# Kernel tuning notes

Hardware: AMD Instinct MI355X
Metric: run time of the kernel (lower is better)

Reference implementation:

```python
import jax, jax.numpy as jnp
import numpy as np

N_HEAD = 16
N_EMBD = 1024
HEAD_DIM = N_EMBD // N_HEAD
ROPE_BASE = 10000.0


def _rope_tables(T, dim):
    inv_freq = 1.0 / (ROPE_BASE ** (jnp.arange(0, dim, 2, dtype=jnp.float32) / dim))
    t = jnp.arange(T, dtype=jnp.float32)
    freqs = jnp.einsum('i,j->ij', t, inv_freq)          # [T, dim/2]
    emb = jnp.concatenate((freqs, freqs), axis=-1)       # [T, dim]
    return jnp.cos(emb), jnp.sin(emb)


def _rotate_half(x):
    x1, x2 = jnp.split(x, 2, axis=-1)
    return jnp.concatenate((-x2, x1), axis=-1)


def setup_inputs() -> dict:
    key = jax.random.key(0)
    k_x, k_wa, k_ba, k_wp, k_bp = jax.random.split(key, 5)
    B, T, C = 2, 2048, N_EMBD
    x = jax.random.normal(k_x, (B, T, C), dtype=jnp.float32)
    # torch Linear weights: [out, in]
    W_attn = jax.random.normal(k_wa, (3 * C, C), dtype=jnp.float32) * (1.0 / np.sqrt(C))
    b_attn = jax.random.normal(k_ba, (3 * C,), dtype=jnp.float32) * 0.01
    W_proj = jax.random.normal(k_wp, (C, C), dtype=jnp.float32) * (1.0 / np.sqrt(C))
    b_proj = jax.random.normal(k_bp, (C,), dtype=jnp.float32) * 0.01
    return {"x": x, "W_attn": W_attn, "b_attn": b_attn, "W_proj": W_proj, "b_proj": b_proj}


def reference(x, W_attn, b_attn, W_proj, b_proj):
    B, T, C = x.shape
    H, D = N_HEAD, HEAD_DIM
    qkv = jnp.einsum('btc,oc->bto', x, W_attn) + b_attn   # [B,T,3C]
    q, k, v = jnp.split(qkv, 3, axis=2)
    # [B,T,C] -> [B,H,T,D]
    q = q.reshape(B, T, H, D).transpose(0, 2, 1, 3)
    k = k.reshape(B, T, H, D).transpose(0, 2, 1, 3)
    v = v.reshape(B, T, H, D).transpose(0, 2, 1, 3)
    cos, sin = _rope_tables(T, D)                          # [T,D]
    q = q * cos + _rotate_half(q) * sin
    k = k * cos + _rotate_half(k) * sin
    att = jnp.einsum('bhqd,bhkd->bhqk', q, k) * (1.0 / np.sqrt(D))
    causal = jnp.tril(jnp.ones((T, T), dtype=bool))
    att = jnp.where(causal, att, -jnp.inf)
    att = jax.nn.softmax(att, axis=-1)
    y = jnp.einsum('bhqk,bhkd->bhqd', att, v)              # [B,H,T,D]
    y = y.transpose(0, 2, 1, 3).reshape(B, T, C)
    y = jnp.einsum('btc,oc->bto', y, W_proj) + b_proj
    return y
```

## Files before the change

kernel.cpp:

```cpp
#include <hip/hip_runtime.h>


typedef unsigned short u16;
typedef u16 u16x4 __attribute__((ext_vector_type(4)));
typedef u16 u16x8 __attribute__((ext_vector_type(8)));
typedef short s16x8 __attribute__((ext_vector_type(8)));
typedef float f32x4 __attribute__((ext_vector_type(4)));

#define T_SEQ 2048
#define C_EMB 1024
#define NH 16
#define HD 64

#define MFMA16(a, b, c) __builtin_amdgcn_mfma_f32_16x16x32_bf16(a, b, c, 0, 0, 0)

__device__ __forceinline__ u16 f2bf(float f) {
    union { float f; unsigned int i; } x; x.f = f;
    unsigned int r = x.i + 0x7fffu + ((x.i >> 16) & 1u);
    return (u16)(r >> 16);
}
__device__ __forceinline__ u16x4 pack4(f32x4 v) {
    u16x4 o;
#pragma unroll
    for (int j = 0; j < 4; ++j) o[j] = f2bf(v[j]);
    return o;
}

__global__ __launch_bounds__(256) void conv_k(const float* __restrict__ src, u16* __restrict__ dst, int n8) {
    int i = blockIdx.x * 256 + threadIdx.x;
    if (i >= n8) return;
    f32x4 a = ((const f32x4*)src)[i * 2];
    f32x4 b = ((const f32x4*)src)[i * 2 + 1];
    u16x8 o;
#pragma unroll
    for (int j = 0; j < 4; ++j) o[j] = f2bf(a[j]);
#pragma unroll
    for (int j = 0; j < 4; ++j) o[4 + j] = f2bf(b[j]);
    ((u16x8*)dst)[i] = o;
}

__global__ __launch_bounds__(256) void rope_tab_k(float2* __restrict__ tab) {
    int idx = blockIdx.x * 256 + threadIdx.x;
    int t = idx >> 5, j = idx & 31;
    float inv = __builtin_exp2f(-0.41524101186092f * (float)j);
    float s_, c_;
    sincosf((float)t * inv, &s_, &c_);
    tab[idx] = make_float2(c_, s_);
}

__global__ __launch_bounds__(256) void qkv_rope_k(const u16* __restrict__ xb, const u16* __restrict__ Wab,
                                                  const float* __restrict__ bias,
                                                  const float2* __restrict__ tab,
                                                  u16* __restrict__ qb, u16* __restrict__ kb,
                                                  u16* __restrict__ vt) {
    __shared__ u16 smem[2 * 128 * 72];
    u16* As = smem;
    u16* Bs = smem + 128 * 72;
    int tid = threadIdx.x;
    int n0 = blockIdx.x * 128, m0 = blockIdx.y * 128;
    int w = tid >> 6, lane = tid & 63, lr = lane & 15, quad = lane >> 4;
    int wr = w >> 1, wc = w & 1;
    f32x4 acc[4][4] = {};
    for (int kt = 0; kt < C_EMB; kt += 64) {
#pragma unroll
        for (int it = 0; it < 4; ++it) {
            int idx = it * 256 + tid;
            int row = idx >> 3, c8 = (idx & 7) << 3;
            *(s16x8*)&As[row * 72 + c8] = *(const s16x8*)(xb + (size_t)(m0 + row) * C_EMB + kt + c8);
            *(s16x8*)&Bs[row * 72 + c8] = *(const s16x8*)(Wab + (size_t)(n0 + row) * C_EMB + kt + c8);
        }
        __syncthreads();
#pragma unroll
        for (int ks = 0; ks < 64; ks += 32) {
            s16x8 af[4], bf[4];
#pragma unroll
            for (int i = 0; i < 4; ++i)
                af[i] = *(const s16x8*)&As[(wr * 64 + i * 16 + lr) * 72 + ks + quad * 8];
#pragma unroll
            for (int j = 0; j < 4; ++j)
                bf[j] = *(const s16x8*)&Bs[(wc * 64 + j * 16 + lr) * 72 + ks + quad * 8];
#pragma unroll
            for (int i = 0; i < 4; ++i)
#pragma unroll
                for (int j = 0; j < 4; ++j) acc[i][j] = MFMA16(af[i], bf[j], acc[i][j]);
        }
        __syncthreads();
    }
    int sec = n0 >> 10;
    float bv[4];
#pragma unroll
    for (int j = 0; j < 4; ++j) bv[j] = bias[n0 + wc * 64 + j * 16 + lr];

    int h0 = (n0 & 1023) >> 6;
    int b = m0 >> 11, tbase = m0 & 2047;
    if (sec == 2) {
        u16* Ct = smem;
#pragma unroll
        for (int i = 0; i < 4; ++i)
#pragma unroll
            for (int j = 0; j < 4; ++j) {
                f32x4 vv;
#pragma unroll
                for (int r = 0; r < 4; ++r) vv[r] = acc[i][j][r] + bv[j];
                int d = wc * 64 + j * 16 + lr;
                int m4 = wr * 64 + i * 16 + quad * 4;
                *(u16x4*)&Ct[d * 136 + m4] = pack4(vv);
            }
        __syncthreads();
        size_t hb = (size_t)(b * NH);
#pragma unroll
        for (int p = 0; p < 8; ++p) {
            int idx = p * 256 + tid;
            int d = idx >> 4, mc = (idx & 15) << 3;
            s16x8 vdat = *(const s16x8*)&Ct[d * 136 + mc];
            int h = h0 + (d >> 6), dd = d & 63;
            *(s16x8*)(vt + ((hb + h) * HD + dd) * T_SEQ + tbase + mc) = vdat;
        }
    } else {
        u16* dst = (sec == 0) ? qb : kb;
        float qs = (sec == 0) ? 0.18033688011112043f : 1.0f;
        u16* Ct = smem;
#pragma unroll
        for (int i = 0; i < 4; ++i)
#pragma unroll
            for (int r = 0; r < 4; ++r) {
                int mrow = wr * 64 + i * 16 + quad * 4 + r;
                int t = (m0 + mrow) & 2047;
#pragma unroll
                for (int j = 0; j < 2; ++j) {
                    int d1 = j * 16 + lr;
                    float2 cs = tab[t * 32 + d1];
                    float v1 = acc[i][j][r] + bv[j];
                    float v2 = acc[i][j + 2][r] + bv[j + 2];
                    int n1 = wc * 64 + j * 16 + lr;
                    Ct[mrow * 136 + n1]      = f2bf((v1 * cs.x - v2 * cs.y) * qs);
                    Ct[mrow * 136 + n1 + 32] = f2bf((v2 * cs.x + v1 * cs.y) * qs);
                }
            }
        __syncthreads();
#pragma unroll
        for (int p = 0; p < 8; ++p) {
            int idx = p * 256 + tid;
            int mrow = idx >> 4, c = idx & 15;
            s16x8 vdat = *(const s16x8*)&Ct[mrow * 136 + c * 8];
            int h = h0 + (c >> 3), dd = (c & 7) << 3;
            *(s16x8*)(dst + ((size_t)(b * NH + h) * T_SEQ + tbase + mrow) * HD + dd) = vdat;
        }
    }
}

__global__ __launch_bounds__(256) void flash_k(const u16* __restrict__ qb, const u16* __restrict__ kb,
                                               const u16* __restrict__ vt, u16* __restrict__ yab) {
    __shared__ u16 Ks[2][64 * 72];
    __shared__ u16 Vs[2][64 * 72];
    __shared__ u16 Ps[4][32 * 72];
    int tid = threadIdx.x;
    int bx = blockIdx.x, by = blockIdx.y;
    int qt = (by < 16) ? (15 - bx) : bx;
    int bh = by;
    int w = tid >> 6, lane = tid & 63, lr = lane & 15, quad = lane >> 4;
    int q0 = qt * 128;
    const u16* qh = qb + (size_t)bh * T_SEQ * HD;
    const u16* kh = kb + (size_t)bh * T_SEQ * HD;
    const u16* vh = vt + (size_t)bh * HD * T_SEQ;

    int rb[2];
    rb[0] = q0 + w * 16;
    rb[1] = q0 + 112 - w * 16;

    s16x8 aq[2][2];
#pragma unroll
    for (int s = 0; s < 2; ++s)
#pragma unroll
        for (int ks = 0; ks < 2; ++ks)
            aq[s][ks] = *(const s16x8*)(qh + (size_t)(rb[s] + lr) * HD + ks * 32 + quad * 8);

    int srow = tid >> 3, sc8 = (tid & 7) << 3;

    float m_i[2] = {-1e30f, -1e30f}, l_i[2] = {0.f, 0.f};
    f32x4 oacc[2][4] = {};

    int ktmax = 2 * qt + 1;
    {
        s16x8 kr0 = *(const s16x8*)(kh + (size_t)srow * HD + sc8);
        s16x8 kr1 = *(const s16x8*)(kh + (size_t)(srow + 32) * HD + sc8);
        s16x8 vr0 = *(const s16x8*)(vh + (size_t)srow * T_SEQ + sc8);
        s16x8 vr1 = *(const s16x8*)(vh + (size_t)(srow + 32) * T_SEQ + sc8);
        *(s16x8*)&Ks[0][srow * 72 + sc8] = kr0;
        *(s16x8*)&Ks[0][(srow + 32) * 72 + sc8] = kr1;
        *(s16x8*)&Vs[0][srow * 72 + sc8] = vr0;
        *(s16x8*)&Vs[0][(srow + 32) * 72 + sc8] = vr1;
    }
    __syncthreads();

    for (int kt = 0; kt <= ktmax; ++kt) {
        int cur = kt & 1;
        int k0 = kt * 64;
        bool pf = kt < ktmax;
        s16x8 kr0, kr1, vr0, vr1;
        if (pf) {
            int kn = k0 + 64;
            kr0 = *(const s16x8*)(kh + (size_t)(kn + srow) * HD + sc8);
            kr1 = *(const s16x8*)(kh + (size_t)(kn + srow + 32) * HD + sc8);
            vr0 = *(const s16x8*)(vh + (size_t)srow * T_SEQ + kn + sc8);
            vr1 = *(const s16x8*)(vh + (size_t)(srow + 32) * T_SEQ + kn + sc8);
        }
        const u16* Kc = Ks[cur];
        const u16* Vc = Vs[cur];
        s16x8 ak[2][4], av[2][4];
#pragma unroll
        for (int ks = 0; ks < 2; ++ks)
#pragma unroll
            for (int tc = 0; tc < 4; ++tc) {
                ak[ks][tc] = *(const s16x8*)&Kc[(tc * 16 + lr) * 72 + ks * 32 + quad * 8];
                av[ks][tc] = *(const s16x8*)&Vc[(tc * 16 + lr) * 72 + ks * 32 + quad * 8];
            }

#pragma unroll
        for (int s = 0; s < 2; ++s) {
            int rbase = rb[s];
            if (k0 > rbase + 15) continue;
            f32x4 sacc[4] = {};
#pragma unroll
            for (int ks = 0; ks < 2; ++ks)
#pragma unroll
                for (int tc = 0; tc < 4; ++tc) sacc[tc] = MFMA16(ak[ks][tc], aq[s][ks], sacc[tc]);
            if (k0 + 63 > rbase) {
#pragma unroll
                for (int tc = 0; tc < 4; ++tc)
#pragma unroll
                    for (int r = 0; r < 4; ++r)
                        if (k0 + tc * 16 + quad * 4 + r > rbase + lr) sacc[tc][r] = -1e30f;
            }
            f32x4 mv = sacc[0];
#pragma unroll
            for (int tc = 1; tc < 4; ++tc)
#pragma unroll
                for (int r = 0; r < 4; ++r) mv[r] = fmaxf(mv[r], sacc[tc][r]);
            float mx = fmaxf(fmaxf(mv[0], mv[1]), fmaxf(mv[2], mv[3]));
            mx = fmaxf(mx, __shfl_xor(mx, 16, 64));
            mx = fmaxf(mx, __shfl_xor(mx, 32, 64));
            float mo = m_i[s];
            bool need = !__all(mx <= mo + 8.0f);
            float alpha = 1.0f;
            if (need) {
                float mn = fmaxf(mo, mx);
                alpha = __builtin_exp2f(mo - mn);
                m_i[s] = mn;
                l_i[s] *= alpha;
            }
            float mnow = m_i[s];
            f32x4 rv = {0.f, 0.f, 0.f, 0.f};
#pragma unroll
            for (int tc = 0; tc < 4; ++tc)
#pragma unroll
                for (int r = 0; r < 4; ++r) {
                    float p = __builtin_exp2f(sacc[tc][r] - mnow);
                    sacc[tc][r] = p;
                    rv[r] += p;
                }
            float rs = (rv[0] + rv[1]) + (rv[2] + rv[3]);
            rs += __shfl_xor(rs, 16, 64);
            rs += __shfl_xor(rs, 32, 64);
            l_i[s] += rs;
#pragma unroll
            for (int tc = 0; tc < 4; ++tc)
                *(u16x4*)&Ps[w][(s * 16 + lr) * 72 + tc * 16 + quad * 4] = pack4(sacc[tc]);
            if (need) {
#pragma unroll
                for (int tn = 0; tn < 4; ++tn)
#pragma unroll
                    for (int r = 0; r < 4; ++r) oacc[s][tn][r] *= alpha;
            }
#pragma unroll
            for (int ks = 0; ks < 2; ++ks) {
                s16x8 ap = *(const s16x8*)&Ps[w][(s * 16 + lr) * 72 + ks * 32 + quad * 8];
#pragma unroll
                for (int tn = 0; tn < 4; ++tn) oacc[s][tn] = MFMA16(av[ks][tn], ap, oacc[s][tn]);
            }
        }
        if (pf) {
            int nx = cur ^ 1;
            *(s16x8*)&Ks[nx][srow * 72 + sc8] = kr0;
            *(s16x8*)&Ks[nx][(srow + 32) * 72 + sc8] = kr1;
            *(s16x8*)&Vs[nx][srow * 72 + sc8] = vr0;
            *(s16x8*)&Vs[nx][(srow + 32) * 72 + sc8] = vr1;
        }
        __syncthreads();
    }
    int b = bh >> 4, hh = bh & 15;
#pragma unroll
    for (int s = 0; s < 2; ++s) {
        float inv = 1.f / l_i[s];
        int t = rb[s] + lr;
        size_t base = ((size_t)b * T_SEQ + t) * C_EMB + hh * HD;
#pragma unroll
        for (int tn = 0; tn < 4; ++tn) {
            f32x4 vv;
#pragma unroll
            for (int r = 0; r < 4; ++r) vv[r] = oacc[s][tn][r] * inv;
            *(u16x4*)(yab + base + tn * 16 + quad * 4) = pack4(vv);
        }
    }
}

__global__ __launch_bounds__(256) void proj_k(const u16* __restrict__ ya, const u16* __restrict__ Wpb,
                                              const float* __restrict__ bias, float* __restrict__ out) {
    __shared__ u16 As[128 * 72];
    __shared__ u16 Bs[128 * 72];
    int tid = threadIdx.x;
    int n0 = blockIdx.x * 128, m0 = blockIdx.y * 128;
    int w = tid >> 6, lane = tid & 63, lr = lane & 15, quad = lane >> 4;
    int wr = w >> 1, wc = w & 1;
    f32x4 acc[4][4] = {};
    for (int kt = 0; kt < C_EMB; kt += 64) {
#pragma unroll
        for (int it = 0; it < 4; ++it) {
            int idx = it * 256 + tid;
            int row = idx >> 3, c8 = (idx & 7) << 3;
            *(s16x8*)&As[row * 72 + c8] = *(const s16x8*)(ya + (size_t)(m0 + row) * C_EMB + kt + c8);
            *(s16x8*)&Bs[row * 72 + c8] = *(const s16x8*)(Wpb + (size_t)(n0 + row) * C_EMB + kt + c8);
        }
        __syncthreads();
#pragma unroll
        for (int ks = 0; ks < 64; ks += 32) {
            s16x8 af[4], bf[4];
#pragma unroll
            for (int i = 0; i < 4; ++i)
                af[i] = *(const s16x8*)&As[(wr * 64 + i * 16 + lr) * 72 + ks + quad * 8];
#pragma unroll
            for (int j = 0; j < 4; ++j)
                bf[j] = *(const s16x8*)&Bs[(wc * 64 + j * 16 + lr) * 72 + ks + quad * 8];
#pragma unroll
            for (int i = 0; i < 4; ++i)
#pragma unroll
                for (int j = 0; j < 4; ++j) acc[i][j] = MFMA16(af[i], bf[j], acc[i][j]);
        }
        __syncthreads();
    }
    float bv[4];
#pragma unroll
    for (int j = 0; j < 4; ++j) bv[j] = bias[n0 + wc * 64 + j * 16 + lr];
#pragma unroll
    for (int i = 0; i < 4; ++i)
#pragma unroll
        for (int r = 0; r < 4; ++r) {
            int m = m0 + wr * 64 + i * 16 + quad * 4 + r;
#pragma unroll
            for (int j = 0; j < 4; ++j)
                out[(size_t)m * C_EMB + n0 + wc * 64 + j * 16 + lr] = acc[i][j][r] + bv[j];
        }
}

extern "C" void kernel_launch(void* const* d_in, const int* in_sizes, int n_in,
                              void* d_out, int out_size, void* d_ws, size_t ws_size,
                              hipStream_t stream) {
    const float *x = nullptr, *Wa = nullptr, *ba = nullptr, *Wp = nullptr, *bp = nullptr;
    for (int i = 0; i < n_in; ++i) {
        switch (in_sizes[i]) {
            case 4194304: x  = (const float*)d_in[i]; break;
            case 3145728: Wa = (const float*)d_in[i]; break;
            case 3072:    ba = (const float*)d_in[i]; break;
            case 1048576: Wp = (const float*)d_in[i]; break;
            case 1024:    bp = (const float*)d_in[i]; break;
            default: break;
        }
    }
    float* out = (float*)d_out;

    char* ws = (char*)d_ws;
    u16* qb     = (u16*)(ws);
    u16* kb     = (u16*)(ws + 8388608);
    u16* vt     = (u16*)(ws + 16777216);
    u16* yab    = (u16*)(ws + 25165824);
    float2* tab = (float2*)(ws + 33554432);
    u16* xb     = (u16*)(ws + 35651584);
    u16* Wab    = (u16*)(ws + 44040192);
    u16* Wpb    = (u16*)(ws + 50331648);

    conv_k<<<2048, 256, 0, stream>>>(x, xb, 524288);
    conv_k<<<1536, 256, 0, stream>>>(Wa, Wab, 393216);
    conv_k<<<512, 256, 0, stream>>>(Wp, Wpb, 131072);
    rope_tab_k<<<256, 256, 0, stream>>>(tab);
    qkv_rope_k<<<dim3(24, 32), 256, 0, stream>>>(xb, Wab, ba, tab, qb, kb, vt);
    flash_k<<<dim3(16, 32), 256, 0, stream>>>(qb, kb, vt, yab);
    proj_k<<<dim3(8, 32), 256, 0, stream>>>(yab, Wpb, bp, out);
}
```

Measured before the change: 222.5 us.

## Split flash attention work across 8 waves, one 16-row strip each

The flash attention block grows from 256 to 512 threads. Each of the 8 waves now owns a single 16-row query strip instead of two mirrored strips per wave, and K/V tile loading is spread over twice as many threads. The aim is more parallelism and lower per-thread register pressure (launch bounds 512,4), which should raise occupancy and latency hiding. In exchange, the causal-balancing row pairing is lost, so waves in the same block get unequal work and lower-row waves idle at barriers while the others finish.

```diff
diff --git a/kernel.cpp b/kernel.cpp
--- a/kernel.cpp
+++ b/kernel.cpp
@@ -149,11 +149,11 @@
     }
 }
 
-__global__ __launch_bounds__(256) void flash_k(const u16* __restrict__ qb, const u16* __restrict__ kb,
-                                               const u16* __restrict__ vt, u16* __restrict__ yab) {
+__global__ __launch_bounds__(512, 4) void flash_k(const u16* __restrict__ qb, const u16* __restrict__ kb,
+                                                  const u16* __restrict__ vt, u16* __restrict__ yab) {
     __shared__ u16 Ks[2][64 * 72];
     __shared__ u16 Vs[2][64 * 72];
-    __shared__ u16 Ps[4][32 * 72];
+    __shared__ u16 Ps[8][16 * 72];
     int tid = threadIdx.x;
     int bx = blockIdx.x, by = blockIdx.y;
     int qt = (by < 16) ? (15 - bx) : bx;
@@ -164,32 +164,24 @@
     const u16* kh = kb + (size_t)bh * T_SEQ * HD;
     const u16* vh = vt + (size_t)bh * HD * T_SEQ;
 
-    int rb[2];
-    rb[0] = q0 + w * 16;
-    rb[1] = q0 + 112 - w * 16;
-
-    s16x8 aq[2][2];
-#pragma unroll
-    for (int s = 0; s < 2; ++s)
-#pragma unroll
-        for (int ks = 0; ks < 2; ++ks)
-            aq[s][ks] = *(const s16x8*)(qh + (size_t)(rb[s] + lr) * HD + ks * 32 + quad * 8);
+    int rbase = q0 + w * 16;
+
+    s16x8 aq[2];
+#pragma unroll
+    for (int ks = 0; ks < 2; ++ks)
+        aq[ks] = *(const s16x8*)(qh + (size_t)(rbase + lr) * HD + ks * 32 + quad * 8);
 
     int srow = tid >> 3, sc8 = (tid & 7) << 3;
 
-    float m_i[2] = {-1e30f, -1e30f}, l_i[2] = {0.f, 0.f};
-    f32x4 oacc[2][4] = {};
+    float m_i = -1e30f, l_i = 0.f;
+    f32x4 oacc[4] = {};
 
     int ktmax = 2 * qt + 1;
     {
         s16x8 kr0 = *(const s16x8*)(kh + (size_t)srow * HD + sc8);
-        s16x8 kr1 = *(const s16x8*)(kh + (size_t)(srow + 32) * HD + sc8);
         s16x8 vr0 = *(const s16x8*)(vh + (size_t)srow * T_SEQ + sc8);
-        s16x8 vr1 = *(const s16x8*)(vh + (size_t)(srow + 32) * T_SEQ + sc8);
         *(s16x8*)&Ks[0][srow * 72 + sc8] = kr0;
-        *(s16x8*)&Ks[0][(srow + 32) * 72 + sc8] = kr1;
         *(s16x8*)&Vs[0][srow * 72 + sc8] = vr0;
-        *(s16x8*)&Vs[0][(srow + 32) * 72 + sc8] = vr1;
     }
     __syncthreads();
 
@@ -197,34 +189,29 @@
         int cur = kt & 1;
         int k0 = kt * 64;
         bool pf = kt < ktmax;
-        s16x8 kr0, kr1, vr0, vr1;
+        s16x8 kr0, vr0;
         if (pf) {
             int kn = k0 + 64;
             kr0 = *(const s16x8*)(kh + (size_t)(kn + srow) * HD + sc8);
-            kr1 = *(const s16x8*)(kh + (size_t)(kn + srow + 32) * HD + sc8);
             vr0 = *(const s16x8*)(vh + (size_t)srow * T_SEQ + kn + sc8);
-            vr1 = *(const s16x8*)(vh + (size_t)(srow + 32) * T_SEQ + kn + sc8);
         }
         const u16* Kc = Ks[cur];
         const u16* Vc = Vs[cur];
-        s16x8 ak[2][4], av[2][4];
-#pragma unroll
-        for (int ks = 0; ks < 2; ++ks)
-#pragma unroll
-            for (int tc = 0; tc < 4; ++tc) {
-                ak[ks][tc] = *(const s16x8*)&Kc[(tc * 16 + lr) * 72 + ks * 32 + quad * 8];
-                av[ks][tc] = *(const s16x8*)&Vc[(tc * 16 + lr) * 72 + ks * 32 + quad * 8];
-            }
-
-#pragma unroll
-        for (int s = 0; s < 2; ++s) {
-            int rbase = rb[s];
-            if (k0 > rbase + 15) continue;
+
+        if (k0 <= rbase + 15) {
+            s16x8 ak[2][4], av[2][4];
+#pragma unroll
+            for (int ks = 0; ks < 2; ++ks)
+#pragma unroll
+                for (int tc = 0; tc < 4; ++tc) {
+                    ak[ks][tc] = *(const s16x8*)&Kc[(tc * 16 + lr) * 72 + ks * 32 + quad * 8];
+                    av[ks][tc] = *(const s16x8*)&Vc[(tc * 16 + lr) * 72 + ks * 32 + quad * 8];
+                }
             f32x4 sacc[4] = {};
 #pragma unroll
             for (int ks = 0; ks < 2; ++ks)
 #pragma unroll
-                for (int tc = 0; tc < 4; ++tc) sacc[tc] = MFMA16(ak[ks][tc], aq[s][ks], sacc[tc]);
+                for (int tc = 0; tc < 4; ++tc) sacc[tc] = MFMA16(ak[ks][tc], aq[ks], sacc[tc]);
             if (k0 + 63 > rbase) {
 #pragma unroll
                 for (int tc = 0; tc < 4; ++tc)
@@ -240,16 +227,16 @@
             float mx = fmaxf(fmaxf(mv[0], mv[1]), fmaxf(mv[2], mv[3]));
             mx = fmaxf(mx, __shfl_xor(mx, 16, 64));
             mx = fmaxf(mx, __shfl_xor(mx, 32, 64));
-            float mo = m_i[s];
+            float mo = m_i;
             bool need = !__all(mx <= mo + 8.0f);
             float alpha = 1.0f;
             if (need) {
                 float mn = fmaxf(mo, mx);
                 alpha = __builtin_exp2f(mo - mn);
-                m_i[s] = mn;
-                l_i[s] *= alpha;
-            }
-            float mnow = m_i[s];
+                m_i = mn;
+                l_i *= alpha;
+            }
+            float mnow = m_i;
             f32x4 rv = {0.f, 0.f, 0.f, 0.f};
 #pragma unroll
             for (int tc = 0; tc < 4; ++tc)
@@ -262,43 +249,40 @@
             float rs = (rv[0] + rv[1]) + (rv[2] + rv[3]);
             rs += __shfl_xor(rs, 16, 64);
             rs += __shfl_xor(rs, 32, 64);
-            l_i[s] += rs;
+            l_i += rs;
 #pragma unroll
             for (int tc = 0; tc < 4; ++tc)
-                *(u16x4*)&Ps[w][(s * 16 + lr) * 72 + tc * 16 + quad * 4] = pack4(sacc[tc]);
+                *(u16x4*)&Ps[w][lr * 72 + tc * 16 + quad * 4] = pack4(sacc[tc]);
             if (need) {
 #pragma unroll
                 for (int tn = 0; tn < 4; ++tn)
 #pragma unroll
-                    for (int r = 0; r < 4; ++r) oacc[s][tn][r] *= alpha;
+                    for (int r = 0; r < 4; ++r) oacc[tn][r] *= alpha;
             }
 #pragma unroll
             for (int ks = 0; ks < 2; ++ks) {
-                s16x8 ap = *(const s16x8*)&Ps[w][(s * 16 + lr) * 72 + ks * 32 + quad * 8];
-#pragma unroll
-                for (int tn = 0; tn < 4; ++tn) oacc[s][tn] = MFMA16(av[ks][tn], ap, oacc[s][tn]);
+                s16x8 ap = *(const s16x8*)&Ps[w][lr * 72 + ks * 32 + quad * 8];
+#pragma unroll
+                for (int tn = 0; tn < 4; ++tn) oacc[tn] = MFMA16(av[ks][tn], ap, oacc[tn]);
             }
         }
         if (pf) {
             int nx = cur ^ 1;
             *(s16x8*)&Ks[nx][srow * 72 + sc8] = kr0;
-            *(s16x8*)&Ks[nx][(srow + 32) * 72 + sc8] = kr1;
             *(s16x8*)&Vs[nx][srow * 72 + sc8] = vr0;
-            *(s16x8*)&Vs[nx][(srow + 32) * 72 + sc8] = vr1;
         }
         __syncthreads();
     }
     int b = bh >> 4, hh = bh & 15;
-#pragma unroll
-    for (int s = 0; s < 2; ++s) {
-        float inv = 1.f / l_i[s];
-        int t = rb[s] + lr;
+    {
+        float inv = 1.f / l_i;
+        int t = rbase + lr;
         size_t base = ((size_t)b * T_SEQ + t) * C_EMB + hh * HD;
 #pragma unroll
         for (int tn = 0; tn < 4; ++tn) {
             f32x4 vv;
 #pragma unroll
-            for (int r = 0; r < 4; ++r) vv[r] = oacc[s][tn][r] * inv;
+            for (int r = 0; r < 4; ++r) vv[r] = oacc[tn][r] * inv;
             *(u16x4*)(yab + base + tn * 16 + quad * 4) = pack4(vv);
         }
     }
@@ -383,6 +367,6 @@
     conv_k<<<512, 256, 0, stream>>>(Wp, Wpb, 131072);
     rope_tab_k<<<256, 256, 0, stream>>>(tab);
     qkv_rope_k<<<dim3(24, 32), 256, 0, stream>>>(xb, Wab, ba, tab, qb, kb, vt);
-    flash_k<<<dim3(16, 32), 256, 0, stream>>>(qb, kb, vt, yab);
+    flash_k<<<dim3(16, 32), 512, 0, stream>>>(qb, kb, vt, yab);
     proj_k<<<dim3(8, 32), 256, 0, stream>>>(yab, Wpb, bp, out);
 }
```

Result: faster. 212.4 us (-4.5%).
